# Optimization experiments

Measured on AMD Instinct MI355X. Metric: run time of the kernel, lower is better.

## Reference

```python
import jax, jax.numpy as jnp
import numpy as np

N_NODES = 50000
N_EDGES = 800000
F_IN = 128
F_OUT = 64


def setup_inputs() -> dict:
    key = jax.random.key(0)
    k_x, k_w, k_r, k_c, k_v = jax.random.split(key, 5)
    x = jax.random.normal(k_x, (N_NODES, F_IN), dtype=jnp.float32)
    weight = jax.random.normal(k_w, (F_IN, F_OUT), dtype=jnp.float32)
    edge_row = jnp.sort(jax.random.randint(k_r, (N_EDGES,), 0, N_NODES, dtype=jnp.int32))
    edge_col = jax.random.randint(k_c, (N_EDGES,), 0, N_NODES, dtype=jnp.int32)
    edge_val = jax.random.uniform(k_v, (N_EDGES,), dtype=jnp.float32)
    return {"x": x, "weight": weight, "edge_row": edge_row,
            "edge_col": edge_col, "edge_val": edge_val}


def reference(x, weight, edge_row, edge_col, edge_val):
    # pre_sup = dot(x, W)                      : [N, F_out] dense GEMM
    pre_sup = x @ weight
    # support @ pre_sup (sparse-dense matmul) via COO gather + segment sum:
    # out[r] = sum_{e: row[e]==r} val[e] * pre_sup[col[e]]
    msgs = edge_val[:, None] * pre_sup[edge_col]          # [E, F_out]
    out = jax.ops.segment_sum(msgs, edge_row, num_segments=N_NODES)
    # act = relu, no bias
    return jax.nn.relu(out)
```

## Files before the change

### kernel.cpp

```cpp
#include <hip/hip_runtime.h>
#include <hip/hip_bf16.h>

#define F_IN 128
#define F_OUT 64

typedef __attribute__((ext_vector_type(8))) short short8;
typedef __attribute__((ext_vector_type(4))) float f32x4;

__device__ __forceinline__ unsigned short f2bf_rne(float f) {
  unsigned int u = __builtin_bit_cast(unsigned int, f);
  u += 0x7fffu + ((u >> 16) & 1u);
  return (unsigned short)(u >> 16);
}
__device__ __forceinline__ float bf_lo(unsigned int u) {
  return __builtin_bit_cast(float, u << 16);
}
__device__ __forceinline__ float bf_hi(unsigned int u) {
  return __builtin_bit_cast(float, u & 0xffff0000u);
}

__global__ __launch_bounds__(256) void gcn_gemm_rowptr(
    const float* __restrict__ x, const float* __restrict__ w,
    unsigned short* __restrict__ pre,
    const int* __restrict__ edge_row, int* __restrict__ row_ptr,
    int n_nodes, int n_edges, int gemm_blocks) {
  const int tid = threadIdx.x;

  if (blockIdx.x >= gemm_blocks) {
    const int r = (blockIdx.x - gemm_blocks) * 256 + tid;
    if (r > n_nodes) return;
    int lo = 0, hi = n_edges;
    while (lo < hi) {
      const int mid = (lo + hi) >> 1;
      if (edge_row[mid] < r) lo = mid + 1; else hi = mid;
    }
    row_ptr[r] = lo;
    return;
  }

  __shared__ __align__(16) unsigned short wt_hi[64 * 128];

  {
#pragma unroll
    for (int i = 0; i < 8; ++i) {
      const int flat4 = tid + i * 256;
      const float4 v = ((const float4*)w)[flat4];
      const float fv[4] = {v.x, v.y, v.z, v.w};
#pragma unroll
      for (int j = 0; j < 4; ++j) {
        const int flat = flat4 * 4 + j;
        const int k = flat >> 6;
        const int n = flat & 63;
        int off = (n << 8) + (k << 1);
        off ^= (n & 7) << 4;
        *(unsigned short*)((char*)wt_hi + off) = f2bf_rne(fv[j]);
      }
    }
  }
  __syncthreads();

  const int lane = tid & 63;
  const int mt = blockIdx.x * 4 + (tid >> 6);
  const int m0 = mt * 16;
  if (m0 >= n_nodes) return;

  const int lrow = lane & 15;
  const int lk = lane >> 4;
  const bool full = (m0 + 16 <= n_nodes);
  const int arow = full ? (m0 + lrow) : min(m0 + lrow, n_nodes - 1);

  f32x4 acc[4];
#pragma unroll
  for (int i = 0; i < 4; ++i) acc[i] = (f32x4){0.f, 0.f, 0.f, 0.f};

#pragma unroll
  for (int ks = 0; ks < 4; ++ks) {
    const float4* xp =
        (const float4*)(x + (size_t)arow * F_IN + ks * 32 + lk * 8);
    const float4 q0 = xp[0];
    const float4 q1 = xp[1];
    const float fv[8] = {q0.x, q0.y, q0.z, q0.w, q1.x, q1.y, q1.z, q1.w};
    short8 ah;
#pragma unroll
    for (int i = 0; i < 8; ++i) ah[i] = (short)f2bf_rne(fv[i]);
#pragma unroll
    for (int nt = 0; nt < 4; ++nt) {
      const int n = nt * 16 + lrow;
      int off = (n << 8) + (ks * 64 + lk * 16);
      off ^= (n & 7) << 4;
      const short8 bh = *(const short8*)((const char*)wt_hi + off);
      acc[nt] = __builtin_amdgcn_mfma_f32_16x16x32_bf16(ah, bh, acc[nt], 0, 0, 0);
    }
  }

#pragma unroll
  for (int nt = 0; nt < 4; ++nt) {
#pragma unroll
    for (int r = 0; r < 4; ++r) {
      const int row = m0 + lk * 4 + r;
      if (full || row < n_nodes)
        pre[(size_t)row * F_OUT + nt * 16 + lrow] = f2bf_rne(acc[nt][r]);
    }
  }
}

__global__ __launch_bounds__(256) void gcn_spmm(
    const unsigned short* __restrict__ pre, const int* __restrict__ row_ptr,
    const int* __restrict__ edge_col, const float* __restrict__ edge_val,
    float* __restrict__ out, int n_nodes) {
  const int lane = threadIdx.x & 63;
  const int q  = lane >> 4;
  const int fl = lane & 15;
  const int wid = (int)((blockIdx.x * blockDim.x + threadIdx.x) >> 6);
  const int rbase = wid * 4;
  if (rbase >= n_nodes) return;

  const int myrow = rbase + q;
  const bool valid = myrow < n_nodes;
  const int rowc = valid ? myrow : n_nodes - 1;
  const int e0 = row_ptr[rowc];
  const int e1 = valid ? row_ptr[rowc + 1] : e0;

  int md = e1 - e0;
  md = max(md, __shfl_xor(md, 16));
  md = max(md, __shfl_xor(md, 32));

  float a0 = 0.f, a1 = 0.f, a2 = 0.f, a3 = 0.f;
  const char* prebase = (const char*)pre + ((size_t)fl << 3);

  for (int sb = 0; sb < md; sb += 16) {
    int myc = 0;
    float myv = 0.f;
    const int ei = e0 + sb + fl;
    if (ei < e1) {
      myc = edge_col[ei] << 7;
      myv = edge_val[ei];
    }
    const int qb = lane & 48;
    int   cc[16];
    float vv[16];
#pragma unroll
    for (int j = 0; j < 16; ++j) {
      cc[j] = __shfl(myc, qb + j);
      vv[j] = __shfl(myv, qb + j);
    }
    uint2 p[16];
#pragma unroll
    for (int j = 0; j < 16; ++j)
      p[j] = *(const uint2*)(prebase + (size_t)(unsigned int)cc[j]);
#pragma unroll
    for (int j = 0; j < 16; ++j) {
      a0 = fmaf(vv[j], bf_lo(p[j].x), a0);
      a1 = fmaf(vv[j], bf_hi(p[j].x), a1);
      a2 = fmaf(vv[j], bf_lo(p[j].y), a2);
      a3 = fmaf(vv[j], bf_hi(p[j].y), a3);
    }
  }

  if (valid) {
    float4 o;
    o.x = fmaxf(a0, 0.f);
    o.y = fmaxf(a1, 0.f);
    o.z = fmaxf(a2, 0.f);
    o.w = fmaxf(a3, 0.f);
    *(float4*)(out + (size_t)myrow * F_OUT + fl * 4) = o;
  }
}

extern "C" void kernel_launch(void* const* d_in, const int* in_sizes, int n_in,
                              void* d_out, int out_size, void* d_ws, size_t ws_size,
                              hipStream_t stream) {
  const float* x        = (const float*)d_in[0];
  const float* w        = (const float*)d_in[1];
  const int*   edge_row = (const int*)d_in[2];
  const int*   edge_col = (const int*)d_in[3];
  const float* edge_val = (const float*)d_in[4];
  float* out = (float*)d_out;

  const int n_nodes = in_sizes[0] / F_IN;
  const int n_edges = in_sizes[2];

  unsigned short* pre = (unsigned short*)d_ws;
  int* row_ptr = (int*)((char*)d_ws +
                        (size_t)n_nodes * F_OUT * sizeof(unsigned short));

  const int m_tiles = (n_nodes + 15) / 16;
  const int gemm_blocks = (m_tiles + 3) / 4;
  const int rp_blocks = (n_nodes + 1 + 255) / 256;
  gcn_gemm_rowptr<<<gemm_blocks + rp_blocks, 256, 0, stream>>>(
      x, w, pre, edge_row, row_ptr, n_nodes, n_edges, gemm_blocks);

  const int spmm_blocks = (n_nodes + 15) / 16;
  gcn_spmm<<<spmm_blocks, 256, 0, stream>>>(pre, row_ptr, edge_col, edge_val,
                                            out, n_nodes);
}
```

Baseline: 33.48 us.

## Quantize intermediate features to int8 per-row with split-bf16 GEMM

The GEMM now runs three bf16 MFMAs per tile (hi*hi, lo*hi, hi*lo) to recover near-fp32 accuracy. Its output is stored as per-row symmetric int8 with a float scale, not bf16. The SpMM gathers 4-byte int8 rows instead of 8-byte bf16 rows, halving gather traffic, and folds the scale into the edge weight. The cost is triple MFMA work, a second LDS weight copy, an extra scale load per edge, and int8 quantization error in the output.

Measured after the change: 37.54 us. 1.12x slower.

```diff
diff --git a/kernel.cpp b/kernel.cpp
--- a/kernel.cpp
+++ b/kernel.cpp
@@ -12,16 +12,13 @@
   u += 0x7fffu + ((u >> 16) & 1u);
   return (unsigned short)(u >> 16);
 }
-__device__ __forceinline__ float bf_lo(unsigned int u) {
-  return __builtin_bit_cast(float, u << 16);
-}
-__device__ __forceinline__ float bf_hi(unsigned int u) {
-  return __builtin_bit_cast(float, u & 0xffff0000u);
+__device__ __forceinline__ float bfu2f(unsigned short u) {
+  return __builtin_bit_cast(float, (unsigned int)u << 16);
 }
 
 __global__ __launch_bounds__(256) void gcn_gemm_rowptr(
     const float* __restrict__ x, const float* __restrict__ w,
-    unsigned short* __restrict__ pre,
+    signed char* __restrict__ pre8, float* __restrict__ scales,
     const int* __restrict__ edge_row, int* __restrict__ row_ptr,
     int n_nodes, int n_edges, int gemm_blocks) {
   const int tid = threadIdx.x;
@@ -39,6 +36,7 @@
   }
 
   __shared__ __align__(16) unsigned short wt_hi[64 * 128];
+  __shared__ __align__(16) unsigned short wt_lo[64 * 128];
 
   {
 #pragma unroll
@@ -53,7 +51,9 @@
         const int n = flat & 63;
         int off = (n << 8) + (k << 1);
         off ^= (n & 7) << 4;
-        *(unsigned short*)((char*)wt_hi + off) = f2bf_rne(fv[j]);
+        const unsigned short h = f2bf_rne(fv[j]);
+        *(unsigned short*)((char*)wt_hi + off) = h;
+        *(unsigned short*)((char*)wt_lo + off) = f2bf_rne(fv[j] - bfu2f(h));
       }
     }
   }
@@ -80,34 +80,53 @@
     const float4 q0 = xp[0];
     const float4 q1 = xp[1];
     const float fv[8] = {q0.x, q0.y, q0.z, q0.w, q1.x, q1.y, q1.z, q1.w};
-    short8 ah;
-#pragma unroll
-    for (int i = 0; i < 8; ++i) ah[i] = (short)f2bf_rne(fv[i]);
+    short8 ah, al;
+#pragma unroll
+    for (int i = 0; i < 8; ++i) {
+      const unsigned short h = f2bf_rne(fv[i]);
+      ah[i] = (short)h;
+      al[i] = (short)f2bf_rne(fv[i] - bfu2f(h));
+    }
 #pragma unroll
     for (int nt = 0; nt < 4; ++nt) {
       const int n = nt * 16 + lrow;
       int off = (n << 8) + (ks * 64 + lk * 16);
       off ^= (n & 7) << 4;
       const short8 bh = *(const short8*)((const char*)wt_hi + off);
+      const short8 bl = *(const short8*)((const char*)wt_lo + off);
       acc[nt] = __builtin_amdgcn_mfma_f32_16x16x32_bf16(ah, bh, acc[nt], 0, 0, 0);
-    }
-  }
-
-#pragma unroll
-  for (int nt = 0; nt < 4; ++nt) {
-#pragma unroll
-    for (int r = 0; r < 4; ++r) {
-      const int row = m0 + lk * 4 + r;
-      if (full || row < n_nodes)
-        pre[(size_t)row * F_OUT + nt * 16 + lrow] = f2bf_rne(acc[nt][r]);
+      acc[nt] = __builtin_amdgcn_mfma_f32_16x16x32_bf16(al, bh, acc[nt], 0, 0, 0);
+      acc[nt] = __builtin_amdgcn_mfma_f32_16x16x32_bf16(ah, bl, acc[nt], 0, 0, 0);
+    }
+  }
+
+#pragma unroll
+  for (int r = 0; r < 4; ++r) {
+    float m = fmaxf(fmaxf(fabsf(acc[0][r]), fabsf(acc[1][r])),
+                    fmaxf(fabsf(acc[2][r]), fabsf(acc[3][r])));
+    m = fmaxf(m, __shfl_xor(m, 1));
+    m = fmaxf(m, __shfl_xor(m, 2));
+    m = fmaxf(m, __shfl_xor(m, 4));
+    m = fmaxf(m, __shfl_xor(m, 8));
+    const float iv = m > 0.f ? 127.0f / m : 0.f;
+    const int row = m0 + lk * 4 + r;
+    if (full || row < n_nodes) {
+      const int q0 = __float2int_rn(acc[0][r] * iv);
+      const int q1 = __float2int_rn(acc[1][r] * iv);
+      const int q2 = __float2int_rn(acc[2][r] * iv);
+      const int q3 = __float2int_rn(acc[3][r] * iv);
+      const unsigned int u = (q0 & 0xff) | ((q1 & 0xff) << 8) |
+                             ((q2 & 0xff) << 16) | ((unsigned)(q3 & 0xff) << 24);
+      *(unsigned int*)(pre8 + (size_t)row * 64 + lrow * 4) = u;
+      if (lrow == 0) scales[row] = m * (1.0f / 127.0f);
     }
   }
 }
 
 __global__ __launch_bounds__(256) void gcn_spmm(
-    const unsigned short* __restrict__ pre, const int* __restrict__ row_ptr,
-    const int* __restrict__ edge_col, const float* __restrict__ edge_val,
-    float* __restrict__ out, int n_nodes) {
+    const signed char* __restrict__ pre8, const float* __restrict__ scales,
+    const int* __restrict__ row_ptr, const int* __restrict__ edge_col,
+    const float* __restrict__ edge_val, float* __restrict__ out, int n_nodes) {
   const int lane = threadIdx.x & 63;
   const int q  = lane >> 4;
   const int fl = lane & 15;
@@ -126,15 +145,16 @@
   md = max(md, __shfl_xor(md, 32));
 
   float a0 = 0.f, a1 = 0.f, a2 = 0.f, a3 = 0.f;
-  const char* prebase = (const char*)pre + ((size_t)fl << 3);
+  const char* pb = (const char*)pre8 + (fl << 2);
 
   for (int sb = 0; sb < md; sb += 16) {
     int myc = 0;
     float myv = 0.f;
     const int ei = e0 + sb + fl;
     if (ei < e1) {
-      myc = edge_col[ei] << 7;
-      myv = edge_val[ei];
+      const int c = edge_col[ei];
+      myv = edge_val[ei] * scales[c];
+      myc = c << 6;
     }
     const int qb = lane & 48;
     int   cc[16];
@@ -144,26 +164,25 @@
       cc[j] = __shfl(myc, qb + j);
       vv[j] = __shfl(myv, qb + j);
     }
-    uint2 p[16];
+    unsigned int p[16];
 #pragma unroll
     for (int j = 0; j < 16; ++j)
-      p[j] = *(const uint2*)(prebase + (size_t)(unsigned int)cc[j]);
+      p[j] = *(const unsigned int*)(pb + (size_t)(unsigned int)cc[j]);
 #pragma unroll
     for (int j = 0; j < 16; ++j) {
-      a0 = fmaf(vv[j], bf_lo(p[j].x), a0);
-      a1 = fmaf(vv[j], bf_hi(p[j].x), a1);
-      a2 = fmaf(vv[j], bf_lo(p[j].y), a2);
-      a3 = fmaf(vv[j], bf_hi(p[j].y), a3);
+      a0 = fmaf(vv[j], (float)((int)(p[j] << 24) >> 24), a0);
+      a1 = fmaf(vv[j], (float)((int)(p[j] << 16) >> 24), a1);
+      a2 = fmaf(vv[j], (float)((int)(p[j] <<  8) >> 24), a2);
+      a3 = fmaf(vv[j], (float)((int)p[j] >> 24), a3);
     }
   }
 
   if (valid) {
-    float4 o;
-    o.x = fmaxf(a0, 0.f);
-    o.y = fmaxf(a1, 0.f);
-    o.z = fmaxf(a2, 0.f);
-    o.w = fmaxf(a3, 0.f);
-    *(float4*)(out + (size_t)myrow * F_OUT + fl * 4) = o;
+    float* ob = out + (size_t)myrow * F_OUT + fl;
+    ob[0]  = fmaxf(a0, 0.f);
+    ob[16] = fmaxf(a1, 0.f);
+    ob[32] = fmaxf(a2, 0.f);
+    ob[48] = fmaxf(a3, 0.f);
   }
 }
 
@@ -180,17 +199,18 @@
   const int n_nodes = in_sizes[0] / F_IN;
   const int n_edges = in_sizes[2];
 
-  unsigned short* pre = (unsigned short*)d_ws;
-  int* row_ptr = (int*)((char*)d_ws +
-                        (size_t)n_nodes * F_OUT * sizeof(unsigned short));
+  signed char* pre8 = (signed char*)d_ws;
+  float* scales = (float*)((char*)d_ws + (size_t)n_nodes * 64);
+  int* row_ptr  = (int*)((char*)d_ws + (size_t)n_nodes * 64 +
+                         (size_t)n_nodes * sizeof(float));
 
   const int m_tiles = (n_nodes + 15) / 16;
   const int gemm_blocks = (m_tiles + 3) / 4;
   const int rp_blocks = (n_nodes + 1 + 255) / 256;
   gcn_gemm_rowptr<<<gemm_blocks + rp_blocks, 256, 0, stream>>>(
-      x, w, pre, edge_row, row_ptr, n_nodes, n_edges, gemm_blocks);
+      x, w, pre8, scales, edge_row, row_ptr, n_nodes, n_edges, gemm_blocks);
 
   const int spmm_blocks = (n_nodes + 15) / 16;
-  gcn_spmm<<<spmm_blocks, 256, 0, stream>>>(pre, row_ptr, edge_col, edge_val,
-                                            out, n_nodes);
-}
+  gcn_spmm<<<spmm_blocks, 256, 0, stream>>>(pre8, scales, row_ptr, edge_col,
+                                            edge_val, out, n_nodes);
+}
```

## Stage block edge metadata in LDS for SpMM gather

Applied to the files above, without the earlier changes.

The SpMM kernel now has each 16-row block cooperatively load the block's contiguous edge range (column index and value) into shared memory in chunks of 1024. Each 16-lane group then reads its row's edges from LDS with an 8-way unrolled loop, replacing the per-wave shuffle broadcast. The aim is coalesced metadata loads and fewer cross-lane shuffles. In exchange it adds block-wide barriers, LDS usage and per-row divergent loop lengths within a wave.

After: 34.30 us. +2.4%, slower.

```diff
diff --git a/kernel.cpp b/kernel.cpp
--- a/kernel.cpp
+++ b/kernel.cpp
@@ -3,6 +3,7 @@
 
 #define F_IN 128
 #define F_OUT 64
+#define CHUNK_EDGES 1024
 
 typedef __attribute__((ext_vector_type(8))) short short8;
 typedef __attribute__((ext_vector_type(4))) float f32x4;
@@ -108,52 +109,66 @@
     const unsigned short* __restrict__ pre, const int* __restrict__ row_ptr,
     const int* __restrict__ edge_col, const float* __restrict__ edge_val,
     float* __restrict__ out, int n_nodes) {
-  const int lane = threadIdx.x & 63;
-  const int q  = lane >> 4;
+  __shared__ uint2 meta[CHUNK_EDGES];
+
+  const int tid = threadIdx.x;
+  const int lane = tid & 63;
+  const int wv = tid >> 6;
+  const int q = lane >> 4;
   const int fl = lane & 15;
-  const int wid = (int)((blockIdx.x * blockDim.x + threadIdx.x) >> 6);
-  const int rbase = wid * 4;
-  if (rbase >= n_nodes) return;
-
-  const int myrow = rbase + q;
+  const int rbase = blockIdx.x * 16;
+
+  const int myrow = rbase + wv * 4 + q;
   const bool valid = myrow < n_nodes;
   const int rowc = valid ? myrow : n_nodes - 1;
-  const int e0 = row_ptr[rowc];
-  const int e1 = valid ? row_ptr[rowc + 1] : e0;
-
-  int md = e1 - e0;
-  md = max(md, __shfl_xor(md, 16));
-  md = max(md, __shfl_xor(md, 32));
+  const int my_e0 = row_ptr[rowc];
+  const int my_e1 = valid ? row_ptr[rowc + 1] : my_e0;
+
+  const int blk_last = min(rbase + 16, n_nodes);
+  const int blk_e0 = row_ptr[rbase];
+  const int blk_e1 = row_ptr[blk_last];
 
   float a0 = 0.f, a1 = 0.f, a2 = 0.f, a3 = 0.f;
-  const char* prebase = (const char*)pre + ((size_t)fl << 3);
-
-  for (int sb = 0; sb < md; sb += 16) {
-    int myc = 0;
-    float myv = 0.f;
-    const int ei = e0 + sb + fl;
-    if (ei < e1) {
-      myc = edge_col[ei] << 7;
-      myv = edge_val[ei];
-    }
-    const int qb = lane & 48;
-    int   cc[16];
-    float vv[16];
-#pragma unroll
-    for (int j = 0; j < 16; ++j) {
-      cc[j] = __shfl(myc, qb + j);
-      vv[j] = __shfl(myv, qb + j);
-    }
-    uint2 p[16];
-#pragma unroll
-    for (int j = 0; j < 16; ++j)
-      p[j] = *(const uint2*)(prebase + (size_t)(unsigned int)cc[j]);
-#pragma unroll
-    for (int j = 0; j < 16; ++j) {
-      a0 = fmaf(vv[j], bf_lo(p[j].x), a0);
-      a1 = fmaf(vv[j], bf_hi(p[j].x), a1);
-      a2 = fmaf(vv[j], bf_lo(p[j].y), a2);
-      a3 = fmaf(vv[j], bf_hi(p[j].y), a3);
+  const char* pb = (const char*)pre + ((size_t)fl << 3);
+
+  for (int ch = blk_e0; ch < blk_e1; ch += CHUNK_EDGES) {
+    const int cend = min(ch + CHUNK_EDGES, blk_e1);
+    const int cnt = cend - ch;
+    if (ch != blk_e0) __syncthreads();
+    for (int i = tid; i < cnt; i += 256)
+      meta[i] = make_uint2((unsigned)edge_col[ch + i] << 7,
+                           __float_as_uint(edge_val[ch + i]));
+    __syncthreads();
+
+    const int s = max(my_e0, ch) - ch;
+    const int t = min(my_e1, cend) - ch;
+
+    int j = s;
+    for (; j + 8 <= t; j += 8) {
+      uint2 m[8];
+#pragma unroll
+      for (int u = 0; u < 8; ++u) m[u] = meta[j + u];
+      uint2 p[8];
+#pragma unroll
+      for (int u = 0; u < 8; ++u)
+        p[u] = *(const uint2*)(pb + (size_t)m[u].x);
+#pragma unroll
+      for (int u = 0; u < 8; ++u) {
+        const float v = __builtin_bit_cast(float, m[u].y);
+        a0 = fmaf(v, bf_lo(p[u].x), a0);
+        a1 = fmaf(v, bf_hi(p[u].x), a1);
+        a2 = fmaf(v, bf_lo(p[u].y), a2);
+        a3 = fmaf(v, bf_hi(p[u].y), a3);
+      }
+    }
+    for (; j < t; ++j) {
+      const uint2 m = meta[j];
+      const uint2 p = *(const uint2*)(pb + (size_t)m.x);
+      const float v = __builtin_bit_cast(float, m.y);
+      a0 = fmaf(v, bf_lo(p.x), a0);
+      a1 = fmaf(v, bf_hi(p.x), a1);
+      a2 = fmaf(v, bf_lo(p.y), a2);
+      a3 = fmaf(v, bf_hi(p.y), a3);
     }
   }
 
```
